# Kernel optimization log

Measured on AMD Instinct MI355X. Metric: run time of the kernel, lower is better.

## Reference

```python
import jax, jax.numpy as jnp
import numpy as np

N_NODES = 50000
N_EDGES = 800000
NUM_GRAPHS = 512


def setup_inputs() -> dict:
    key = jax.random.key(0)
    ks = jax.random.split(key, 8)
    x = jax.random.normal(ks[0], (N_NODES, 128), dtype=jnp.float32)
    W1 = jax.random.normal(ks[1], (128, 128), dtype=jnp.float32) * (1.0 / np.sqrt(128))
    b1 = jnp.zeros((128,), dtype=jnp.float32)
    W2 = jax.random.normal(ks[2], (128, 64), dtype=jnp.float32) * (1.0 / np.sqrt(128))
    b2 = jnp.zeros((64,), dtype=jnp.float32)
    edge_index = jax.random.randint(ks[3], (2, N_EDGES), 0, N_NODES, dtype=jnp.int32)
    batch = jnp.sort(jax.random.randint(ks[4], (N_NODES,), 0, NUM_GRAPHS, dtype=jnp.int32))
    return {"x": x, "W1": W1, "b1": b1, "W2": W2, "b2": b2,
            "edge_index": edge_index, "batch": batch}


def reference(x, W1, b1, W2, b2, edge_index, batch):
    N = x.shape[0]
    # add self-loops (PyG GCNConv default)
    loop = jnp.arange(N, dtype=edge_index.dtype)
    src = jnp.concatenate([edge_index[0], loop])  # [E+N] message sources (x_j)
    dst = jnp.concatenate([edge_index[1], loop])  # [E+N] aggregation targets
    # symmetric degree normalization: deg^{-1/2}[src] * deg^{-1/2}[dst]
    deg = jax.ops.segment_sum(jnp.ones_like(dst, dtype=x.dtype), dst, num_segments=N)
    dinv = jnp.where(deg > 0, jax.lax.rsqrt(jnp.maximum(deg, 1.0)), 0.0)
    norm = (dinv[src] * dinv[dst])[:, None]  # [E+N, 1]

    def gcn_conv(h, W, b):
        hw = h @ W                                    # [N, d_out]
        msg = hw[src] * norm                          # gather + scale, [E+N, d_out]
        return jax.ops.segment_sum(msg, dst, num_segments=N) + b

    h = jax.nn.relu(gcn_conv(x, W1, b1))
    z = gcn_conv(h, W2, b2)
    # global_mean_pool over batch segment ids
    sums = jax.ops.segment_sum(z, batch, num_segments=NUM_GRAPHS)
    cnt = jax.ops.segment_sum(jnp.ones((N,), z.dtype), batch, num_segments=NUM_GRAPHS)
    return sums / jnp.maximum(cnt, 1.0)[:, None]
```

## Files before the change

kernel.cpp:

```cpp
#include <hip/hip_runtime.h>
#include <hip/hip_fp16.h>


typedef _Float16 half8 __attribute__((ext_vector_type(8)));
typedef float    f32x4 __attribute__((ext_vector_type(4)));
union U4H8 { uint4 u; half8 h; };

__global__ void count_kernel(const int* __restrict__ ei, int E, int N,
                             int* __restrict__ cnt) {
    int i = blockIdx.x * blockDim.x + threadIdx.x;
    if (i >= E + N) return;
    int d = (i < E) ? ei[E + i] : (i - E);
    atomicAdd(&cnt[d], 1);
}

__global__ void scan_block_kernel(const int* __restrict__ cnt, int N,
                                  int* __restrict__ excl, int* __restrict__ partial) {
    __shared__ int tmp[1024];
    int t = threadIdx.x;
    int i = blockIdx.x * 1024 + t;
    int v = (i < N) ? cnt[i] : 0;
    tmp[t] = v;
    __syncthreads();
    for (int off = 1; off < 1024; off <<= 1) {
        int add = (t >= off) ? tmp[t - off] : 0;
        __syncthreads();
        tmp[t] += add;
        __syncthreads();
    }
    if (i < N) excl[i] = tmp[t] - v;
    if (t == 1023) partial[blockIdx.x] = tmp[1023];
}

__global__ void scan_partial_kernel(int* __restrict__ partial, int nb) {
    if (blockIdx.x == 0 && threadIdx.x == 0) {
        int run = 0;
        for (int i = 0; i < nb; ++i) { int v = partial[i]; partial[i] = run; run += v; }
    }
}

__global__ void finalize_kernel(int* __restrict__ indptr, int* __restrict__ cursor,
                                const int* __restrict__ cnt, float* __restrict__ dinv,
                                const int* __restrict__ partial, int N, int total) {
    int i = blockIdx.x * blockDim.x + threadIdx.x;
    if (i < N) {
        int v = indptr[i] + partial[i >> 10];
        indptr[i] = v;
        cursor[i] = v;
        dinv[i] = rsqrtf((float)cnt[i]);
    }
    if (i == 0) indptr[N] = total;
}

__global__ void fill_kernel(const int* __restrict__ ei, int E, int N,
                            int* __restrict__ cursor, const float* __restrict__ dinv,
                            int2* __restrict__ csr_e) {
    int i = blockIdx.x * blockDim.x + threadIdx.x;
    if (i >= E + N) return;
    int s, d;
    if (i < E) { s = ei[i]; d = ei[E + i]; }
    else       { s = i - E; d = s; }
    int pos = atomicAdd(&cursor[d], 1);
    float w = dinv[s] * dinv[d];
    csr_e[pos] = make_int2(s, __float_as_int(w));
}

__global__ void wt_prep_kernel(const float* __restrict__ W1, const float* __restrict__ W2,
                               __half* __restrict__ wt1, __half* __restrict__ wt2) {
    int id = blockIdx.x * blockDim.x + threadIdx.x;
    const float* W; __half* dst; int M_, n, c8;
    if (id < 2048)      { W = W1; dst = wt1; M_ = 128; n = id >> 4;          c8 = id & 15; }
    else if (id < 3072) { W = W2; dst = wt2; M_ = 64;  n = (id - 2048) >> 4; c8 = id & 15; }
    else return;
    union { __half h[8]; uint4 u; } pk;
#pragma unroll
    for (int j = 0; j < 8; ++j) pk.h[j] = __float2half(W[(c8 * 8 + j) * M_ + n]);
    *(uint4*)((char*)dst + n * 256 + ((c8 ^ (n & 15)) << 4)) = pk.u;
}

template<int M, bool HALF_IN>
__global__ __launch_bounds__(256) void gemm_mfma_kernel(const void* __restrict__ Xv,
                                                        const __half* __restrict__ wt,
                                                        __half* __restrict__ out, int NT) {
    __shared__ __align__(16) char wlds[M * 256];
    int tid = threadIdx.x;
    {
        const uint4* src = (const uint4*)wt;
        uint4* dstv = (uint4*)wlds;
#pragma unroll
        for (int i = 0; i < (M * 16) / 256; ++i) dstv[tid + i * 256] = src[tid + i * 256];
    }
    __syncthreads();

    int wid  = tid >> 6;
    int lane = tid & 63;
    int rt   = blockIdx.x * 4 + wid;
    if (rt >= NT) return;
    int l15 = lane & 15, l4 = lane >> 4;

    half8 a[4];
    if (HALF_IN) {
        const char* X = (const char*)Xv;
        size_t rb = (size_t)(rt * 16 + l15) * 256;
#pragma unroll
        for (int c = 0; c < 4; ++c) {
            U4H8 u; u.u = *(const uint4*)(X + rb + c * 64 + l4 * 16);
            a[c] = u.h;
        }
    } else {
        const float* X = (const float*)Xv;
        size_t rb = (size_t)(rt * 16 + l15) * 128;
#pragma unroll
        for (int c = 0; c < 4; ++c) {
            const float* p = X + rb + c * 32 + l4 * 8;
            float4 f0 = *(const float4*)p;
            float4 f1 = *(const float4*)(p + 4);
            half8 h;
            h[0] = (_Float16)f0.x; h[1] = (_Float16)f0.y;
            h[2] = (_Float16)f0.z; h[3] = (_Float16)f0.w;
            h[4] = (_Float16)f1.x; h[5] = (_Float16)f1.y;
            h[6] = (_Float16)f1.z; h[7] = (_Float16)f1.w;
            a[c] = h;
        }
    }

    constexpr int CT = M / 16;
    f32x4 acc[CT];
#pragma unroll
    for (int t = 0; t < CT; ++t) acc[t] = (f32x4){0.f, 0.f, 0.f, 0.f};

#pragma unroll
    for (int c = 0; c < 4; ++c) {
#pragma unroll
        for (int t = 0; t < CT; ++t) {
            int n  = t * 16 + l15;
            int c8 = c * 4 + l4;
            U4H8 b; b.u = *(const uint4*)(wlds + n * 256 + ((c8 ^ (n & 15)) << 4));
            acc[t] = __builtin_amdgcn_mfma_f32_16x16x32_f16(a[c], b.h, acc[t], 0, 0, 0);
        }
    }

#pragma unroll
    for (int t = 0; t < CT; ++t) {
#pragma unroll
        for (int r = 0; r < 4; ++r) {
            int row = rt * 16 + l4 * 4 + r;
            out[(size_t)row * M + t * 16 + l15] = __float2half(acc[t][r]);
        }
    }
}

__device__ __forceinline__ void acc_h8(f32x4& a0, f32x4& a1, uint4 r, float w) {
    __half2* h = (__half2*)&r;
    float2 f0 = __half22float2(h[0]);
    float2 f1 = __half22float2(h[1]);
    float2 f2 = __half22float2(h[2]);
    float2 f3 = __half22float2(h[3]);
    a0[0] = fmaf(f0.x, w, a0[0]); a0[1] = fmaf(f0.y, w, a0[1]);
    a0[2] = fmaf(f1.x, w, a0[2]); a0[3] = fmaf(f1.y, w, a0[3]);
    a1[0] = fmaf(f2.x, w, a1[0]); a1[1] = fmaf(f2.y, w, a1[1]);
    a1[2] = fmaf(f3.x, w, a1[2]); a1[3] = fmaf(f3.y, w, a1[3]);
}

__global__ void agg128_relu_kernel(const uint4* __restrict__ hw,
                                   const int* __restrict__ indptr,
                                   const int2* __restrict__ csr_e,
                                   const float* __restrict__ b1,
                                   uint4* __restrict__ outh, int N) {
    int gid  = (blockIdx.x * blockDim.x + threadIdx.x) >> 4;
    int lane = threadIdx.x & 15;
    if (gid >= N) return;
    int beg = indptr[gid], end = indptr[gid + 1];
    f32x4 a0 = (f32x4){0.f, 0.f, 0.f, 0.f};
    f32x4 a1 = (f32x4){0.f, 0.f, 0.f, 0.f};
    int e = beg;
    for (; e + 4 <= end; e += 4) {
        int2 q0 = csr_e[e], q1 = csr_e[e + 1], q2 = csr_e[e + 2], q3 = csr_e[e + 3];
        uint4 r0 = hw[(size_t)q0.x * 16 + lane];
        uint4 r1 = hw[(size_t)q1.x * 16 + lane];
        uint4 r2 = hw[(size_t)q2.x * 16 + lane];
        uint4 r3 = hw[(size_t)q3.x * 16 + lane];
        acc_h8(a0, a1, r0, __int_as_float(q0.y));
        acc_h8(a0, a1, r1, __int_as_float(q1.y));
        acc_h8(a0, a1, r2, __int_as_float(q2.y));
        acc_h8(a0, a1, r3, __int_as_float(q3.y));
    }
    for (; e < end; ++e) {
        int2 q = csr_e[e];
        uint4 r = hw[(size_t)q.x * 16 + lane];
        acc_h8(a0, a1, r, __int_as_float(q.y));
    }
    float4 b0 = *(const float4*)(b1 + lane * 8);
    float4 b1v = *(const float4*)(b1 + lane * 8 + 4);
    float o0 = fmaxf(a0[0] + b0.x, 0.f), o1 = fmaxf(a0[1] + b0.y, 0.f);
    float o2 = fmaxf(a0[2] + b0.z, 0.f), o3 = fmaxf(a0[3] + b0.w, 0.f);
    float o4 = fmaxf(a1[0] + b1v.x, 0.f), o5 = fmaxf(a1[1] + b1v.y, 0.f);
    float o6 = fmaxf(a1[2] + b1v.z, 0.f), o7 = fmaxf(a1[3] + b1v.w, 0.f);
    __half2 p0 = __floats2half2_rn(o0, o1);
    __half2 p1 = __floats2half2_rn(o2, o3);
    __half2 p2 = __floats2half2_rn(o4, o5);
    __half2 p3 = __floats2half2_rn(o6, o7);
    uint4 pk;
    pk.x = *(unsigned int*)&p0; pk.y = *(unsigned int*)&p1;
    pk.z = *(unsigned int*)&p2; pk.w = *(unsigned int*)&p3;
    outh[(size_t)gid * 16 + lane] = pk;
}

__global__ void agg64_kernel(const uint4* __restrict__ hw,
                             const int* __restrict__ indptr,
                             const int2* __restrict__ csr_e,
                             float* __restrict__ outz, int N) {
    int gid  = (blockIdx.x * blockDim.x + threadIdx.x) >> 3;
    int lane = threadIdx.x & 7;
    if (gid >= N) return;
    int beg = indptr[gid], end = indptr[gid + 1];
    f32x4 a0 = (f32x4){0.f, 0.f, 0.f, 0.f};
    f32x4 a1 = (f32x4){0.f, 0.f, 0.f, 0.f};
    int e = beg;
    for (; e + 4 <= end; e += 4) {
        int2 q0 = csr_e[e], q1 = csr_e[e + 1], q2 = csr_e[e + 2], q3 = csr_e[e + 3];
        uint4 r0 = hw[(size_t)q0.x * 8 + lane];
        uint4 r1 = hw[(size_t)q1.x * 8 + lane];
        uint4 r2 = hw[(size_t)q2.x * 8 + lane];
        uint4 r3 = hw[(size_t)q3.x * 8 + lane];
        acc_h8(a0, a1, r0, __int_as_float(q0.y));
        acc_h8(a0, a1, r1, __int_as_float(q1.y));
        acc_h8(a0, a1, r2, __int_as_float(q2.y));
        acc_h8(a0, a1, r3, __int_as_float(q3.y));
    }
    for (; e < end; ++e) {
        int2 q = csr_e[e];
        uint4 r = hw[(size_t)q.x * 8 + lane];
        acc_h8(a0, a1, r, __int_as_float(q.y));
    }
    float* zp = outz + (size_t)gid * 64 + lane * 8;
    *(f32x4*)zp       = a0;
    *(f32x4*)(zp + 4) = a1;
}

__device__ __forceinline__ int lower_bound_i(const int* a, int n, int key) {
    int lo = 0, hi = n;
    while (lo < hi) {
        int mid = (lo + hi) >> 1;
        if (a[mid] < key) lo = mid + 1; else hi = mid;
    }
    return lo;
}

__global__ void pool_kernel(const float* __restrict__ z, const int* __restrict__ batch,
                            const float* __restrict__ b2, float* __restrict__ out,
                            int N, int G) {
    __shared__ float red[4][64];
    int g  = blockIdx.x;
    int c  = threadIdx.x & 63;
    int rr = threadIdx.x >> 6;
    int s  = lower_bound_i(batch, N, g);
    int e  = lower_bound_i(batch, N, g + 1);
    float acc = 0.f;
    for (int n = s + rr; n < e; n += 4) acc += z[n * 64 + c];
    red[rr][c] = acc;
    __syncthreads();
    if (rr == 0) {
        float a = red[0][c] + red[1][c] + red[2][c] + red[3][c];
        int cnt = e - s;
        out[g * 64 + c] = (cnt > 0) ? (a / (float)cnt + b2[c]) : 0.f;
    }
}

extern "C" void kernel_launch(void* const* d_in, const int* in_sizes, int n_in,
                              void* d_out, int out_size, void* d_ws, size_t ws_size,
                              hipStream_t stream) {
    const float* x  = (const float*)d_in[0];
    const float* W1 = (const float*)d_in[1];
    const float* b1 = (const float*)d_in[2];
    const float* W2 = (const float*)d_in[3];
    const float* b2 = (const float*)d_in[4];
    const int*   ei = (const int*)d_in[5];
    const int*   batch = (const int*)d_in[6];

    const int N = in_sizes[6];
    const int E = in_sizes[5] / 2;
    const int Gnum = out_size / 64;
    const int total = E + N;

    char* ws = (char*)d_ws;
    size_t off = 0;
    auto alloc = [&](size_t bytes) {
        size_t o = off;
        off = (off + bytes + 255) & ~(size_t)255;
        return (void*)(ws + o);
    };
    int*    cnt     = (int*)   alloc((size_t)N * 4);
    int*    indptr  = (int*)   alloc((size_t)(N + 1) * 4);
    int*    cursor  = (int*)   alloc((size_t)N * 4);
    float*  dinv    = (float*) alloc((size_t)N * 4);
    int*    partial = (int*)   alloc(256 * 4);
    int2*   csr_e   = (int2*)  alloc((size_t)total * 8);
    __half* wt1     = (__half*)alloc(128 * 256);
    __half* wt2     = (__half*)alloc(64 * 256);
    __half* bufA    = (__half*)alloc((size_t)N * 128 * 2);
    __half* bufB    = (__half*)alloc((size_t)N * 128 * 2);
    float*  bufZ    = (float*) alloc((size_t)N * 64 * 4);
    (void)ws_size; (void)n_in;

    hipMemsetAsync(cnt, 0, (size_t)N * 4, stream);

    int tb = 256;
    int eg = (total + tb - 1) / tb;
    count_kernel<<<eg, tb, 0, stream>>>(ei, E, N, cnt);
    wt_prep_kernel<<<12, 256, 0, stream>>>(W1, W2, wt1, wt2);

    int nb = (N + 1023) / 1024;
    scan_block_kernel<<<nb, 1024, 0, stream>>>(cnt, N, indptr, partial);
    scan_partial_kernel<<<1, 1, 0, stream>>>(partial, nb);
    finalize_kernel<<<(N + tb - 1) / tb, tb, 0, stream>>>(indptr, cursor, cnt, dinv,
                                                          partial, N, total);
    fill_kernel<<<eg, tb, 0, stream>>>(ei, E, N, cursor, dinv, csr_e);

    const int NT = (N + 15) / 16;
    gemm_mfma_kernel<128, false><<<(NT + 3) / 4, 256, 0, stream>>>(x, wt1, bufA, NT);
    agg128_relu_kernel<<<(N * 16 + 255) / 256, 256, 0, stream>>>(
        (const uint4*)bufA, indptr, csr_e, b1, (uint4*)bufB, N);

    gemm_mfma_kernel<64, true><<<(NT + 3) / 4, 256, 0, stream>>>(bufB, wt2, bufA, NT);
    agg64_kernel<<<(N * 8 + 255) / 256, 256, 0, stream>>>(
        (const uint4*)bufA, indptr, csr_e, bufZ, N);

    pool_kernel<<<Gnum, 256, 0, stream>>>(bufZ, batch, b2, (float*)d_out, N, Gnum);
}
```

Measured before the change: 255.9 us.

## Compress CSR to 16-bit source indices and compute edge weights on the fly

The CSR edge array shrinks from int2 (source index plus precomputed float weight) to a single ushort source index. Both aggregation kernels now rebuild the normalisation weight as dinv[src]*dinv[dst], and the fill kernel no longer reads dinv. This cuts the CSR bytes written during fill and read by the two aggregations, in exchange for an extra small, cache-resident dinv gather per edge. The count and weight-transpose kernels are also merged into one launch. The 16-bit index only works while N stays below 65536, which holds for this problem size.

```diff
diff --git a/kernel.cpp b/kernel.cpp
--- a/kernel.cpp
+++ b/kernel.cpp
@@ -6,12 +6,26 @@
 typedef float    f32x4 __attribute__((ext_vector_type(4)));
 union U4H8 { uint4 u; half8 h; };
 
-__global__ void count_kernel(const int* __restrict__ ei, int E, int N,
-                             int* __restrict__ cnt) {
+__global__ void count_wt_kernel(const int* __restrict__ ei, int E, int N,
+                                int* __restrict__ cnt,
+                                const float* __restrict__ W1, const float* __restrict__ W2,
+                                __half* __restrict__ wt1, __half* __restrict__ wt2) {
     int i = blockIdx.x * blockDim.x + threadIdx.x;
-    if (i >= E + N) return;
-    int d = (i < E) ? ei[E + i] : (i - E);
-    atomicAdd(&cnt[d], 1);
+    int total = E + N;
+    if (i < total) {
+        int d = (i < E) ? ei[E + i] : (i - E);
+        atomicAdd(&cnt[d], 1);
+        return;
+    }
+    int id = i - total;
+    const float* W; __half* dst; int M_, n, c8;
+    if (id < 2048)      { W = W1; dst = wt1; M_ = 128; n = id >> 4;          c8 = id & 15; }
+    else if (id < 3072) { W = W2; dst = wt2; M_ = 64;  n = (id - 2048) >> 4; c8 = id & 15; }
+    else return;
+    union { __half h[8]; uint4 u; } pk;
+#pragma unroll
+    for (int j = 0; j < 8; ++j) pk.h[j] = __float2half(W[(c8 * 8 + j) * M_ + n]);
+    *(uint4*)((char*)dst + n * 256 + ((c8 ^ (n & 15)) << 4)) = pk.u;
 }
 
 __global__ void scan_block_kernel(const int* __restrict__ cnt, int N,
@@ -53,29 +67,14 @@
 }
 
 __global__ void fill_kernel(const int* __restrict__ ei, int E, int N,
-                            int* __restrict__ cursor, const float* __restrict__ dinv,
-                            int2* __restrict__ csr_e) {
+                            int* __restrict__ cursor, ushort* __restrict__ csr) {
     int i = blockIdx.x * blockDim.x + threadIdx.x;
     if (i >= E + N) return;
     int s, d;
     if (i < E) { s = ei[i]; d = ei[E + i]; }
     else       { s = i - E; d = s; }
     int pos = atomicAdd(&cursor[d], 1);
-    float w = dinv[s] * dinv[d];
-    csr_e[pos] = make_int2(s, __float_as_int(w));
-}
-
-__global__ void wt_prep_kernel(const float* __restrict__ W1, const float* __restrict__ W2,
-                               __half* __restrict__ wt1, __half* __restrict__ wt2) {
-    int id = blockIdx.x * blockDim.x + threadIdx.x;
-    const float* W; __half* dst; int M_, n, c8;
-    if (id < 2048)      { W = W1; dst = wt1; M_ = 128; n = id >> 4;          c8 = id & 15; }
-    else if (id < 3072) { W = W2; dst = wt2; M_ = 64;  n = (id - 2048) >> 4; c8 = id & 15; }
-    else return;
-    union { __half h[8]; uint4 u; } pk;
-#pragma unroll
-    for (int j = 0; j < 8; ++j) pk.h[j] = __float2half(W[(c8 * 8 + j) * M_ + n]);
-    *(uint4*)((char*)dst + n * 256 + ((c8 ^ (n & 15)) << 4)) = pk.u;
+    csr[pos] = (ushort)s;
 }
 
 template<int M, bool HALF_IN>
@@ -164,31 +163,36 @@
 
 __global__ void agg128_relu_kernel(const uint4* __restrict__ hw,
                                    const int* __restrict__ indptr,
-                                   const int2* __restrict__ csr_e,
+                                   const ushort* __restrict__ csr,
+                                   const float* __restrict__ dinv,
                                    const float* __restrict__ b1,
                                    uint4* __restrict__ outh, int N) {
     int gid  = (blockIdx.x * blockDim.x + threadIdx.x) >> 4;
     int lane = threadIdx.x & 15;
     if (gid >= N) return;
     int beg = indptr[gid], end = indptr[gid + 1];
+    float dl = dinv[gid];
     f32x4 a0 = (f32x4){0.f, 0.f, 0.f, 0.f};
     f32x4 a1 = (f32x4){0.f, 0.f, 0.f, 0.f};
     int e = beg;
     for (; e + 4 <= end; e += 4) {
-        int2 q0 = csr_e[e], q1 = csr_e[e + 1], q2 = csr_e[e + 2], q3 = csr_e[e + 3];
-        uint4 r0 = hw[(size_t)q0.x * 16 + lane];
-        uint4 r1 = hw[(size_t)q1.x * 16 + lane];
-        uint4 r2 = hw[(size_t)q2.x * 16 + lane];
-        uint4 r3 = hw[(size_t)q3.x * 16 + lane];
-        acc_h8(a0, a1, r0, __int_as_float(q0.y));
-        acc_h8(a0, a1, r1, __int_as_float(q1.y));
-        acc_h8(a0, a1, r2, __int_as_float(q2.y));
-        acc_h8(a0, a1, r3, __int_as_float(q3.y));
+        int s0 = csr[e], s1 = csr[e + 1], s2 = csr[e + 2], s3 = csr[e + 3];
+        float w0 = dinv[s0] * dl, w1 = dinv[s1] * dl;
+        float w2 = dinv[s2] * dl, w3 = dinv[s3] * dl;
+        uint4 r0 = hw[(size_t)s0 * 16 + lane];
+        uint4 r1 = hw[(size_t)s1 * 16 + lane];
+        uint4 r2 = hw[(size_t)s2 * 16 + lane];
+        uint4 r3 = hw[(size_t)s3 * 16 + lane];
+        acc_h8(a0, a1, r0, w0);
+        acc_h8(a0, a1, r1, w1);
+        acc_h8(a0, a1, r2, w2);
+        acc_h8(a0, a1, r3, w3);
     }
     for (; e < end; ++e) {
-        int2 q = csr_e[e];
-        uint4 r = hw[(size_t)q.x * 16 + lane];
-        acc_h8(a0, a1, r, __int_as_float(q.y));
+        int s0 = csr[e];
+        float w0 = dinv[s0] * dl;
+        uint4 r0 = hw[(size_t)s0 * 16 + lane];
+        acc_h8(a0, a1, r0, w0);
     }
     float4 b0 = *(const float4*)(b1 + lane * 8);
     float4 b1v = *(const float4*)(b1 + lane * 8 + 4);
@@ -208,30 +212,35 @@
 
 __global__ void agg64_kernel(const uint4* __restrict__ hw,
                              const int* __restrict__ indptr,
-                             const int2* __restrict__ csr_e,
+                             const ushort* __restrict__ csr,
+                             const float* __restrict__ dinv,
                              float* __restrict__ outz, int N) {
     int gid  = (blockIdx.x * blockDim.x + threadIdx.x) >> 3;
     int lane = threadIdx.x & 7;
     if (gid >= N) return;
     int beg = indptr[gid], end = indptr[gid + 1];
+    float dl = dinv[gid];
     f32x4 a0 = (f32x4){0.f, 0.f, 0.f, 0.f};
     f32x4 a1 = (f32x4){0.f, 0.f, 0.f, 0.f};
     int e = beg;
     for (; e + 4 <= end; e += 4) {
-        int2 q0 = csr_e[e], q1 = csr_e[e + 1], q2 = csr_e[e + 2], q3 = csr_e[e + 3];
-        uint4 r0 = hw[(size_t)q0.x * 8 + lane];
-        uint4 r1 = hw[(size_t)q1.x * 8 + lane];
-        uint4 r2 = hw[(size_t)q2.x * 8 + lane];
-        uint4 r3 = hw[(size_t)q3.x * 8 + lane];
-        acc_h8(a0, a1, r0, __int_as_float(q0.y));
-        acc_h8(a0, a1, r1, __int_as_float(q1.y));
-        acc_h8(a0, a1, r2, __int_as_float(q2.y));
-        acc_h8(a0, a1, r3, __int_as_float(q3.y));
+        int s0 = csr[e], s1 = csr[e + 1], s2 = csr[e + 2], s3 = csr[e + 3];
+        float w0 = dinv[s0] * dl, w1 = dinv[s1] * dl;
+        float w2 = dinv[s2] * dl, w3 = dinv[s3] * dl;
+        uint4 r0 = hw[(size_t)s0 * 8 + lane];
+        uint4 r1 = hw[(size_t)s1 * 8 + lane];
+        uint4 r2 = hw[(size_t)s2 * 8 + lane];
+        uint4 r3 = hw[(size_t)s3 * 8 + lane];
+        acc_h8(a0, a1, r0, w0);
+        acc_h8(a0, a1, r1, w1);
+        acc_h8(a0, a1, r2, w2);
+        acc_h8(a0, a1, r3, w3);
     }
     for (; e < end; ++e) {
-        int2 q = csr_e[e];
-        uint4 r = hw[(size_t)q.x * 8 + lane];
-        acc_h8(a0, a1, r, __int_as_float(q.y));
+        int s0 = csr[e];
+        float w0 = dinv[s0] * dl;
+        uint4 r0 = hw[(size_t)s0 * 8 + lane];
+        acc_h8(a0, a1, r0, w0);
     }
     float* zp = outz + (size_t)gid * 64 + lane * 8;
     *(f32x4*)zp       = a0;
@@ -295,7 +304,7 @@
     int*    cursor  = (int*)   alloc((size_t)N * 4);
     float*  dinv    = (float*) alloc((size_t)N * 4);
     int*    partial = (int*)   alloc(256 * 4);
-    int2*   csr_e   = (int2*)  alloc((size_t)total * 8);
+    ushort* csr     = (ushort*)alloc((size_t)total * 2);
     __half* wt1     = (__half*)alloc(128 * 256);
     __half* wt2     = (__half*)alloc(64 * 256);
     __half* bufA    = (__half*)alloc((size_t)N * 128 * 2);
@@ -306,25 +315,24 @@
     hipMemsetAsync(cnt, 0, (size_t)N * 4, stream);
 
     int tb = 256;
-    int eg = (total + tb - 1) / tb;
-    count_kernel<<<eg, tb, 0, stream>>>(ei, E, N, cnt);
-    wt_prep_kernel<<<12, 256, 0, stream>>>(W1, W2, wt1, wt2);
+    int cg = (total + 3072 + tb - 1) / tb;
+    count_wt_kernel<<<cg, tb, 0, stream>>>(ei, E, N, cnt, W1, W2, wt1, wt2);
 
     int nb = (N + 1023) / 1024;
     scan_block_kernel<<<nb, 1024, 0, stream>>>(cnt, N, indptr, partial);
     scan_partial_kernel<<<1, 1, 0, stream>>>(partial, nb);
     finalize_kernel<<<(N + tb - 1) / tb, tb, 0, stream>>>(indptr, cursor, cnt, dinv,
                                                           partial, N, total);
-    fill_kernel<<<eg, tb, 0, stream>>>(ei, E, N, cursor, dinv, csr_e);
+    fill_kernel<<<(total + tb - 1) / tb, tb, 0, stream>>>(ei, E, N, cursor, csr);
 
     const int NT = (N + 15) / 16;
     gemm_mfma_kernel<128, false><<<(NT + 3) / 4, 256, 0, stream>>>(x, wt1, bufA, NT);
     agg128_relu_kernel<<<(N * 16 + 255) / 256, 256, 0, stream>>>(
-        (const uint4*)bufA, indptr, csr_e, b1, (uint4*)bufB, N);
+        (const uint4*)bufA, indptr, csr, dinv, b1, (uint4*)bufB, N);
 
     gemm_mfma_kernel<64, true><<<(NT + 3) / 4, 256, 0, stream>>>(bufB, wt2, bufA, NT);
     agg64_kernel<<<(N * 8 + 255) / 256, 256, 0, stream>>>(
-        (const uint4*)bufA, indptr, csr_e, bufZ, N);
+        (const uint4*)bufA, indptr, csr, dinv, bufZ, N);
 
     pool_kernel<<<Gnum, 256, 0, stream>>>(bufZ, batch, b2, (float*)d_out, N, Gnum);
 }
```

Result: faster. 243.3 us (-4.9%).
